# Kernel optimization log

Hardware: AMD Instinct MI355X
Metric: run time of the kernel (lower is better)

## Reference

```python
import jax, jax.numpy as jnp
import numpy as np

HEADS = 20
HEAD_DIM = 64  # 1280 // 20
NUM_STYLE_TOKENS = 4
FU_SCALE = 0.5
STYLE_SCALE = 1.0
SCALE = np.float32(1.0 / np.sqrt(HEAD_DIM))


def setup_inputs() -> dict:
    key = jax.random.key(0)
    ks = jax.random.split(key, 9)
    B, S, D_MODEL, D_CROSS, T = 4, 4096, 1280, 768, 77
    sd_m = np.float32(1.0 / np.sqrt(D_MODEL))
    sd_c = np.float32(1.0 / np.sqrt(D_CROSS))
    return {
        "hidden_states": jax.random.normal(ks[0], (B, S, D_MODEL), jnp.float32),
        "encoder_hidden_states": jax.random.normal(ks[1], (B, T + NUM_STYLE_TOKENS, D_CROSS), jnp.float32),
        "Wq": jax.random.normal(ks[2], (D_MODEL, D_MODEL), jnp.float32) * sd_m,
        "Wk": jax.random.normal(ks[3], (D_CROSS, D_MODEL), jnp.float32) * sd_c,
        "Wv": jax.random.normal(ks[4], (D_CROSS, D_MODEL), jnp.float32) * sd_c,
        "Wk_ip": jax.random.normal(ks[5], (D_CROSS, D_MODEL), jnp.float32) * sd_c,
        "Wv_ip": jax.random.normal(ks[6], (D_CROSS, D_MODEL), jnp.float32) * sd_c,
        "Wo": jax.random.normal(ks[7], (D_MODEL, D_MODEL), jnp.float32) * sd_m,
        "bo": jnp.zeros((D_MODEL,), jnp.float32),
    }


def _split_heads(x, B):
    # [B, L, H*D] -> [B, H, L, D]
    return x.reshape(B, -1, HEADS, HEAD_DIM).transpose(0, 2, 1, 3)


def _attn_blend(q, k, v):
    # Manual QK^T softmax with cross-batch prob blending (fuAttn / fuIPAttn).
    probs = jax.nn.softmax(jnp.einsum('bhsd,bhtd->bhst', q, k) * SCALE, axis=-1)
    probs = probs.at[1].set(FU_SCALE * probs[1] + (1.0 - FU_SCALE) * probs[0])
    probs = probs.at[3].set(FU_SCALE * probs[3] + (1.0 - FU_SCALE) * probs[2])
    return jnp.einsum('bhst,bhtd->bhsd', probs, v)


def reference(hidden_states, encoder_hidden_states, Wq, Wk, Wv, Wk_ip, Wv_ip, Wo, bo):
    B, S, _ = hidden_states.shape
    end_pos = encoder_hidden_states.shape[1] - NUM_STYLE_TOKENS
    text = encoder_hidden_states[:, :end_pos, :]       # [B, 77, Dc]
    ip_style = encoder_hidden_states[:, end_pos:, :]   # [B, 4, Dc]

    q = _split_heads(hidden_states @ Wq, B)   # [B,H,S,D]
    k = _split_heads(text @ Wk, B)            # [B,H,77,D]
    v = _split_heads(text @ Wv, B)

    hid = _attn_blend(q, k, v).transpose(0, 2, 1, 3).reshape(B, S, -1)
    raw = hid

    ip_k = _split_heads(ip_style @ Wk_ip, B)  # [B,H,4,D]
    ip_v = _split_heads(ip_style @ Wv_ip, B)
    ip_hid = _attn_blend(q, ip_k, ip_v).transpose(0, 2, 1, 3).reshape(B, S, -1)

    hid = hid + STYLE_SCALE * ip_hid
    # batch rows 0 and 2 keep the raw (text-only) attention output
    hid = hid.at[0].set(raw[0]).at[2].set(raw[2])

    return hid @ Wo + bo
```

## Files before the change

kernel.cpp:

```cpp
#include <hip/hip_runtime.h>
#include <hip/hip_bf16.h>

typedef _Float16 half8 __attribute__((ext_vector_type(8)));
typedef _Float16 half4 __attribute__((ext_vector_type(4)));
typedef float floatx4 __attribute__((ext_vector_type(4)));

#define HEADS_ 20
#define B_    4
#define S_    4096
#define DM    1280
#define DC    768
#define TTOK  77
#define NST   4
#define EROWS 81
#define MROWS 324
#define NT_K  20

__device__ inline void gload_lds16(const void* g, void* l) {
  __builtin_amdgcn_global_load_lds((const __attribute__((address_space(1))) void*)g,
                                   (__attribute__((address_space(3))) void*)l, 16, 0, 0);
}

__global__ __launch_bounds__(256) void cast_f16(const float* __restrict__ in,
                                                _Float16* __restrict__ out, long n) {
  long i = ((long)blockIdx.x * 256 + threadIdx.x) * 8L;
  long stride = (long)gridDim.x * 256 * 8;
  for (; i < n; i += stride) {
    float4 a = *(const float4*)(in + i);
    float4 b = *(const float4*)(in + i + 4);
    half8 h;
    h[0] = (_Float16)a.x; h[1] = (_Float16)a.y; h[2] = (_Float16)a.z; h[3] = (_Float16)a.w;
    h[4] = (_Float16)b.x; h[5] = (_Float16)b.y; h[6] = (_Float16)b.z; h[7] = (_Float16)b.w;
    *(half8*)(out + i) = h;
  }
}

struct TParams { const float* in[6]; _Float16* out[6]; int R[6]; };

__global__ __launch_bounds__(256) void transpose_cast6(TParams p) {
  const int z = blockIdx.z;
  const int R = p.R[z];
  const int r0 = blockIdx.y * 32, c0 = blockIdx.x * 32;
  if (r0 >= R) return;
  const float* __restrict__ in = p.in[z];
  _Float16* __restrict__ out = p.out[z];
  __shared__ float t[32][33];
  int tx = threadIdx.x & 31, ty = threadIdx.x >> 5;
  #pragma unroll
  for (int j = 0; j < 32; j += 8)
    t[ty + j][tx] = in[(size_t)(r0 + ty + j) * DM + c0 + tx];
  __syncthreads();
  #pragma unroll
  for (int j = 0; j < 32; j += 8)
    out[(size_t)(c0 + ty + j) * R + r0 + tx] = (_Float16)t[tx][ty + j];
}

struct Ptrs4 { const _Float16* B[4]; _Float16* C[4]; };

__global__ __launch_bounds__(256) void gemm_kv(const _Float16* __restrict__ A,
                                               Ptrs4 p4, int M, int K, int N) {
  const int tid = threadIdx.x, lane = tid & 63, w = tid >> 6;
  const _Float16* Bp = p4.B[blockIdx.z];
  _Float16* Ch = p4.C[blockIdx.z];
  const int bm = blockIdx.x, bn = blockIdx.y;

  __shared__ _Float16 As[128 * 32];
  __shared__ _Float16 Bs[128 * 32];

  const int wr = (w >> 1) * 64, wc = (w & 1) * 64;
  const int arow = wr + (lane & 15), brow = wc + (lane & 15);
  const int koff = (lane >> 4) * 8;
  floatx4 acc[4][4] = {};

  const int nk = K >> 5;
  for (int kt = 0; kt < nk; ++kt) {
    #pragma unroll
    for (int c = 0; c < 2; ++c) {
      int l16 = w * 64 + lane + c * 256;
      int row = l16 >> 2, kc = (l16 & 3) << 3;
      int gr = bm * 128 + row; if (gr > M - 1) gr = M - 1;
      gload_lds16(A + (size_t)gr * K + kt * 32 + kc, &As[(w + c * 4) * 512]);
      int grb = bn * 128 + row;
      gload_lds16(Bp + (size_t)grb * K + kt * 32 + kc, &Bs[(w + c * 4) * 512]);
    }
    __syncthreads();
    half8 af[4], bf[4];
    #pragma unroll
    for (int m = 0; m < 4; m++) af[m] = *(const half8*)&As[(arow + m * 16) * 32 + koff];
    #pragma unroll
    for (int n = 0; n < 4; n++) bf[n] = *(const half8*)&Bs[(brow + n * 16) * 32 + koff];
    #pragma unroll
    for (int m = 0; m < 4; m++)
      #pragma unroll
      for (int n = 0; n < 4; n++)
        acc[m][n] = __builtin_amdgcn_mfma_f32_16x16x32_f16(af[m], bf[n], acc[m][n], 0, 0, 0);
    __syncthreads();
  }

  const int r0 = (lane >> 4) * 4, c0 = lane & 15;
  #pragma unroll
  for (int m = 0; m < 4; m++) {
    #pragma unroll
    for (int r = 0; r < 4; r++) {
      int grow = bm * 128 + wr + m * 16 + r0 + r;
      if (grow >= M) continue;
      size_t base = (size_t)grow * N + bn * 128 + wc + c0;
      #pragma unroll
      for (int n = 0; n < 4; n++) Ch[base + n * 16] = (_Float16)acc[m][n][r];
    }
  }
}

template<int OMODE>
__global__ __launch_bounds__(256, 2)
void gemm8(const _Float16* __restrict__ A,
           const _Float16* __restrict__ B,
           void* __restrict__ Cout,
           const float* __restrict__ bias) {
  __shared__ _Float16 lds[36864];
  _Float16* const A0 = lds;
  _Float16* const A1 = lds + 8192;
  _Float16* const B0 = lds + 16384;
  _Float16* const B1 = lds + 26624;

  const int tid = threadIdx.x, lane = tid & 63, w = tid >> 6;
  const int swz = (blockIdx.x & 7) * 128 + (blockIdx.x >> 3);
  const int bm = swz >> 3, bn = swz & 7;

  const int wr = w >> 1, wc = w & 1;
  const int ql = lane & 15, lg = lane >> 4, xr = ql & 7;
  const int Abase = (wr * 64 + ql) * 64;
  const int Bbase = (wc * 80 + ql) * 64;

  const int srow = tid >> 3, sslot = tid & 7;
  const int scol = ((sslot ^ (srow & 7)) << 3);
  const _Float16* const Asrc = A + (size_t)(bm * 128 + srow) * DM + scol;
  const _Float16* const Bsrc = B + (size_t)(bn * 160 + srow) * DM + scol;
  const int ldst = w * 512;

  auto stage = [&](const _Float16* src, _Float16* buf, int q, int kt) {
    gload_lds16(src + (size_t)q * 32 * DM + kt * 64, buf + q * 2048 + ldst);
  };
  auto rdA = [&](const _Float16* buf, int m, int ks) -> half8 {
    return *(const half8*)(buf + Abase + m * 1024 + (((ks * 4 + lg) ^ xr) << 3));
  };
  auto rdB = [&](const _Float16* buf, int n, int ks) -> half8 {
    return *(const half8*)(buf + Bbase + n * 1024 + (((ks * 4 + lg) ^ xr) << 3));
  };

  floatx4 acc[4][5] = {};
  half8 bF[5], bG[5], aF[4], aG[4];

  #pragma unroll
  for (int q = 0; q < 4; ++q) stage(Asrc, A0, q, 0);
  #pragma unroll
  for (int q = 0; q < 5; ++q) stage(Bsrc, B0, q, 0);

  auto tile_body = [&](const _Float16* Ac, const _Float16* Bc,
                       _Float16* An, _Float16* Bn, int j, bool pref) {
    if (pref) {
      #pragma unroll
      for (int q = 0; q < 4; ++q) stage(Asrc, An, q, j + 1);
      #pragma unroll
      for (int q = 0; q < 5; ++q) stage(Bsrc, Bn, q, j + 1);
      asm volatile("s_waitcnt vmcnt(9)" ::: "memory");
    } else {
      asm volatile("s_waitcnt vmcnt(0)" ::: "memory");
    }
    asm volatile("s_waitcnt lgkmcnt(0)" ::: "memory");
    __builtin_amdgcn_sched_barrier(0);
    __builtin_amdgcn_s_barrier();
    __builtin_amdgcn_sched_barrier(0);

    #pragma unroll
    for (int n = 0; n < 5; ++n) bF[n] = rdB(Bc, n, 0);
    #pragma unroll
    for (int m = 0; m < 4; ++m) aF[m] = rdA(Ac, m, 0);
    #pragma unroll
    for (int m = 0; m < 4; ++m) {
      if (m == 0) { aG[0] = rdA(Ac, 0, 1); aG[1] = rdA(Ac, 1, 1); }
      if (m == 1) { aG[2] = rdA(Ac, 2, 1); aG[3] = rdA(Ac, 3, 1); bG[0] = rdB(Bc, 0, 1); }
      if (m == 2) { bG[1] = rdB(Bc, 1, 1); bG[2] = rdB(Bc, 2, 1); }
      if (m == 3) { bG[3] = rdB(Bc, 3, 1); bG[4] = rdB(Bc, 4, 1); }
      __builtin_amdgcn_s_setprio(1);
      #pragma unroll
      for (int n = 0; n < 5; ++n)
        acc[m][n] = __builtin_amdgcn_mfma_f32_16x16x32_f16(aF[m], bF[n], acc[m][n], 0, 0, 0);
      __builtin_amdgcn_s_setprio(0);
    }
    #pragma unroll
    for (int m = 0; m < 4; ++m) {
      __builtin_amdgcn_s_setprio(1);
      #pragma unroll
      for (int n = 0; n < 5; ++n)
        acc[m][n] = __builtin_amdgcn_mfma_f32_16x16x32_f16(aG[m], bG[n], acc[m][n], 0, 0, 0);
      __builtin_amdgcn_s_setprio(0);
    }
  };

  for (int j = 0; j < NT_K; j += 2) {
    tile_body(A0, B0, A1, B1, j, true);
    tile_body(A1, B1, A0, B0, j + 1, j + 2 < NT_K);
  }

  const int r0 = lg * 4;
  if constexpr (OMODE == 1) {
    _Float16* Ch = (_Float16*)Cout;
    #pragma unroll
    for (int m = 0; m < 4; ++m)
      #pragma unroll
      for (int r = 0; r < 4; ++r) {
        size_t base = (size_t)(bm * 128 + wr * 64 + m * 16 + r0 + r) * DM + bn * 160 + wc * 80 + ql;
        #pragma unroll
        for (int n = 0; n < 5; ++n)
          Ch[base + n * 16] = (_Float16)(acc[m][n][r] * 0.125f);
      }
  } else {
    float* Cf = (float*)Cout;
    float bv[5];
    #pragma unroll
    for (int n = 0; n < 5; ++n) bv[n] = bias[bn * 160 + wc * 80 + n * 16 + ql];
    #pragma unroll
    for (int m = 0; m < 4; ++m)
      #pragma unroll
      for (int r = 0; r < 4; ++r) {
        size_t base = (size_t)(bm * 128 + wr * 64 + m * 16 + r0 + r) * DM + bn * 160 + wc * 80 + ql;
        #pragma unroll
        for (int n = 0; n < 5; ++n)
          Cf[base + n * 16] = acc[m][n][r] + bv[n];
      }
  }
}

template<bool ODD>
__global__ __launch_bounds__(256) void attn_kernel(const _Float16* __restrict__ Q,
                                                   const _Float16* __restrict__ kf,
                                                   const _Float16* __restrict__ vf,
                                                   const _Float16* __restrict__ ipk,
                                                   const _Float16* __restrict__ ipv,
                                                   _Float16* __restrict__ hid) {
  const int tid = threadIdx.x;
  const int h = blockIdx.y;
  const int b = blockIdx.z * 2 + (ODD ? 1 : 0);
  constexpr bool odd = ODD;
  const int hoff = h * 64;
  const int lane = tid & 63, w = tid >> 6;
  const int g = lane >> 4, ql = lane & 15;

  __shared__ _Float16 K1s[96 * 64];
  __shared__ _Float16 K2s[ODD ? 96 * 64 : 8];
  __shared__ _Float16 VTs[64 * 104];
  __shared__ char Pl[4][16 * 208];
  char* const K1c = (char*)K1s;
  char* const K2c = (char*)K2s;
  char* const VTc = (char*)VTs;
  char* const Pwc = Pl[w];

  const half8 zero8 = {};
  for (int i = tid; i < 96 * 8; i += 256) {
    int key = i >> 3, hb = i & 7;
    int dst = (key * 128 + hb * 16) ^ ((key & 7) << 4);
    half8 v = zero8;
    if (key < TTOK)
      v = *(const half8*)(kf + (size_t)(b * EROWS + key) * DM + hoff + hb * 8);
    else if (odd && key >= 80 && key < 84)
      v = *(const half8*)(ipk + (size_t)(b * EROWS + key - 3) * DM + hoff + hb * 8);
    *(half8*)(K1c + dst) = v;
    if (odd) {
      half8 v2 = zero8;
      if (key < TTOK)
        v2 = *(const half8*)(kf + (size_t)((b - 1) * EROWS + key) * DM + hoff + hb * 8);
      else if (key >= 80 && key < 84)
        v2 = *(const half8*)(ipk + (size_t)((b - 1) * EROWS + key - 3) * DM + hoff + hb * 8);
      *(half8*)(K2c + dst) = v2;
    }
  }
  for (int i = tid; i < 96 * 8; i += 256) {
    int key = i >> 3, hb = i & 7;
    half8 v = zero8;
    if (key < TTOK)
      v = *(const half8*)(vf + (size_t)(b * EROWS + key) * DM + hoff + hb * 8);
    else if (odd && key >= 80 && key < 84)
      v = *(const half8*)(ipv + (size_t)(b * EROWS + key - 3) * DM + hoff + hb * 8);
    #pragma unroll
    for (int e = 0; e < 8; ++e) VTs[(hb * 8 + e) * 104 + key] = v[e];
  }
  __syncthreads();

  for (int t = 0; t < 4; ++t) {
    const int tq0 = blockIdx.x * 256 + t * 64 + w * 16;

    const _Float16* qp = Q + (size_t)(b * S_ + tq0 + ql) * DM + hoff + g * 8;
    half8 bq0 = *(const half8*)(qp);
    half8 bq1 = *(const half8*)(qp + 32);
    half8 bq20 = zero8, bq21 = zero8;
    if (odd) {
      const _Float16* qp2 = Q + (size_t)((b - 1) * S_ + tq0 + ql) * DM + hoff + g * 8;
      bq20 = *(const half8*)(qp2);
      bq21 = *(const half8*)(qp2 + 32);
    }

    floatx4 sA[6], sB[6];
    #pragma unroll
    for (int f = 0; f < (ODD ? 6 : 5); ++f) {
      int key = f * 16 + ql;
      int sw = (key & 7) << 4;
      half8 a0 = *(const half8*)(K1c + ((key * 128 + g * 16) ^ sw));
      half8 a1 = *(const half8*)(K1c + ((key * 128 + g * 16 + 64) ^ sw));
      floatx4 z = {};
      sA[f] = __builtin_amdgcn_mfma_f32_16x16x32_f16(a0, bq0, z, 0, 0, 0);
      sA[f] = __builtin_amdgcn_mfma_f32_16x16x32_f16(a1, bq1, sA[f], 0, 0, 0);
    }
    if (odd) {
      #pragma unroll
      for (int f = 0; f < 6; ++f) {
        int key = f * 16 + ql;
        int sw = (key & 7) << 4;
        half8 a0 = *(const half8*)(K2c + ((key * 128 + g * 16) ^ sw));
        half8 a1 = *(const half8*)(K2c + ((key * 128 + g * 16 + 64) ^ sw));
        floatx4 z = {};
        sB[f] = __builtin_amdgcn_mfma_f32_16x16x32_f16(a0, bq20, z, 0, 0, 0);
        sB[f] = __builtin_amdgcn_mfma_f32_16x16x32_f16(a1, bq21, sB[f], 0, 0, 0);
      }
    }

    const int kb = g * 4;
    float mA = -1e30f;
    #pragma unroll
    for (int f = 0; f < 4; ++f)
      #pragma unroll
      for (int r = 0; r < 4; ++r) mA = fmaxf(mA, sA[f][r]);
    #pragma unroll
    for (int r = 0; r < 4; ++r) if (kb + r <= 12) mA = fmaxf(mA, sA[4][r]);
    mA = fmaxf(mA, __shfl_xor(mA, 16));
    mA = fmaxf(mA, __shfl_xor(mA, 32));
    float lA = 0.f;
    #pragma unroll
    for (int f = 0; f < 4; ++f)
      #pragma unroll
      for (int r = 0; r < 4; ++r) { float e = __expf(sA[f][r] - mA); sA[f][r] = e; lA += e; }
    #pragma unroll
    for (int r = 0; r < 4; ++r) {
      float e = (kb + r <= 12) ? __expf(sA[4][r] - mA) : 0.f;
      sA[4][r] = e; lA += e;
    }
    lA += __shfl_xor(lA, 16);
    lA += __shfl_xor(lA, 32);

    float mB = -1e30f, lB = 0.f, invB = 0.f, invIpA = 0.f, invIpB = 0.f;
    if (odd) {
      #pragma unroll
      for (int f = 0; f < 4; ++f)
        #pragma unroll
        for (int r = 0; r < 4; ++r) mB = fmaxf(mB, sB[f][r]);
      #pragma unroll
      for (int r = 0; r < 4; ++r) if (kb + r <= 12) mB = fmaxf(mB, sB[4][r]);
      mB = fmaxf(mB, __shfl_xor(mB, 16));
      mB = fmaxf(mB, __shfl_xor(mB, 32));
      #pragma unroll
      for (int f = 0; f < 4; ++f)
        #pragma unroll
        for (int r = 0; r < 4; ++r) { float e = __expf(sB[f][r] - mB); sB[f][r] = e; lB += e; }
      #pragma unroll
      for (int r = 0; r < 4; ++r) {
        float e = (kb + r <= 12) ? __expf(sB[4][r] - mB) : 0.f;
        sB[4][r] = e; lB += e;
      }
      lB += __shfl_xor(lB, 16);
      lB += __shfl_xor(lB, 32);
      invB = 0.5f / lB;

      float mia = fmaxf(fmaxf(sA[5][0], sA[5][1]), fmaxf(sA[5][2], sA[5][3]));
      float mib = fmaxf(fmaxf(sB[5][0], sB[5][1]), fmaxf(sB[5][2], sB[5][3]));
      float lia = 0.f, lib = 0.f;
      #pragma unroll
      for (int r = 0; r < 4; ++r) {
        float ea = __expf(sA[5][r] - mia); sA[5][r] = ea; lia += ea;
        float eb = __expf(sB[5][r] - mib); sB[5][r] = eb; lib += eb;
      }
      invIpA = 0.5f / lia;
      invIpB = 0.5f / lib;
    }
    const float invA = (odd ? 0.5f : 1.0f) / lA;

    asm volatile("s_waitcnt lgkmcnt(0)" ::: "memory");
    __builtin_amdgcn_sched_barrier(0);
    #pragma unroll
    for (int f = 0; f < 6; ++f) {
      #pragma unroll
      for (int r = 0; r < 4; ++r) {
        int key = f * 16 + g * 4 + r;
        float p;
        if (f < 5) p = odd ? (sA[f][r] * invA + sB[f][r] * invB) : (sA[f][r] * invA);
        else p = (odd && g == 0) ? (sA[5][r] * invIpA + sB[5][r] * invIpB) : 0.f;
        *(_Float16*)(Pwc + ql * 208 + key * 2) = (_Float16)p;
      }
    }
    asm volatile("s_waitcnt lgkmcnt(0)" ::: "memory");
    __builtin_amdgcn_sched_barrier(0);

    half8 pf[3];
    #pragma unroll
    for (int kf2 = 0; kf2 < 3; ++kf2)
      pf[kf2] = *(const half8*)(Pwc + ql * 208 + g * 16 + kf2 * 64);
    floatx4 acc_o[4] = {};
    #pragma unroll
    for (int dt = 0; dt < 4; ++dt)
      #pragma unroll
      for (int kf2 = 0; kf2 < 3; ++kf2) {
        half8 vfr = *(const half8*)(VTc + (dt * 16 + ql) * 208 + g * 16 + kf2 * 64);
        acc_o[dt] = __builtin_amdgcn_mfma_f32_16x16x32_f16(vfr, pf[kf2], acc_o[dt], 0, 0, 0);
      }

    _Float16* hr = hid + (size_t)(b * S_ + tq0 + ql) * DM + hoff;
    #pragma unroll
    for (int dt = 0; dt < 4; ++dt) {
      half4 hv;
      #pragma unroll
      for (int r = 0; r < 4; ++r) hv[r] = (_Float16)acc_o[dt][r];
      *(half4*)(hr + dt * 16 + g * 4) = hv;
    }
  }
}

extern "C" void kernel_launch(void* const* d_in, const int* in_sizes, int n_in,
                              void* d_out, int out_size, void* d_ws, size_t ws_size,
                              hipStream_t stream) {
  const float* hs   = (const float*)d_in[0];
  const float* ehs  = (const float*)d_in[1];
  const float* Wq   = (const float*)d_in[2];
  const float* Wk   = (const float*)d_in[3];
  const float* Wv   = (const float*)d_in[4];
  const float* Wkip = (const float*)d_in[5];
  const float* Wvip = (const float*)d_in[6];
  const float* Wo   = (const float*)d_in[7];
  const float* bo   = (const float*)d_in[8];
  float* out = (float*)d_out;

  char* ws = (char*)d_ws;
  size_t off = 0;
  auto alloc = [&](size_t bytes) {
    void* p = ws + off;
    off += (bytes + 255) & ~(size_t)255;
    return p;
  };
  _Float16* hs16   = (_Float16*)alloc(20971520UL * 2);
  _Float16* ehs16  = (_Float16*)alloc(248832UL * 2);
  _Float16* WqT    = (_Float16*)alloc(1638400UL * 2);
  _Float16* WoT    = (_Float16*)alloc(1638400UL * 2);
  _Float16* WkT    = (_Float16*)alloc(983040UL * 2);
  _Float16* WvT    = (_Float16*)alloc(983040UL * 2);
  _Float16* WkipT  = (_Float16*)alloc(983040UL * 2);
  _Float16* WvipT  = (_Float16*)alloc(983040UL * 2);
  _Float16* Q16    = (_Float16*)alloc(20971520UL * 2);
  _Float16* kf16   = (_Float16*)alloc(324UL * 1280 * 2);
  _Float16* vf16   = (_Float16*)alloc(324UL * 1280 * 2);
  _Float16* ipkf16 = (_Float16*)alloc(324UL * 1280 * 2);
  _Float16* ipvf16 = (_Float16*)alloc(324UL * 1280 * 2);
  _Float16* hid16 = hs16;

  cast_f16<<<2048, 256, 0, stream>>>(hs, hs16, 20971520L);
  cast_f16<<<128, 256, 0, stream>>>(ehs, ehs16, 248832L);

  TParams tp;
  tp.in[0] = Wq;   tp.out[0] = WqT;   tp.R[0] = 1280;
  tp.in[1] = Wo;   tp.out[1] = WoT;   tp.R[1] = 1280;
  tp.in[2] = Wk;   tp.out[2] = WkT;   tp.R[2] = 768;
  tp.in[3] = Wv;   tp.out[3] = WvT;   tp.R[3] = 768;
  tp.in[4] = Wkip; tp.out[4] = WkipT; tp.R[4] = 768;
  tp.in[5] = Wvip; tp.out[5] = WvipT; tp.R[5] = 768;
  transpose_cast6<<<dim3(40, 40, 6), 256, 0, stream>>>(tp);

  Ptrs4 p4;
  p4.B[0] = WkT; p4.B[1] = WvT; p4.B[2] = WkipT; p4.B[3] = WvipT;
  p4.C[0] = kf16; p4.C[1] = vf16; p4.C[2] = ipkf16; p4.C[3] = ipvf16;

  gemm_kv<<<dim3(3, 10, 4), 256, 0, stream>>>(ehs16, p4, MROWS, DC, DM);
  gemm8<1><<<1024, 256, 0, stream>>>(hs16, WqT, (void*)Q16, nullptr);
  attn_kernel<false><<<dim3(16, 20, 2), 256, 0, stream>>>(Q16, kf16, vf16, ipkf16, ipvf16, hid16);
  attn_kernel<true><<<dim3(16, 20, 2), 256, 0, stream>>>(Q16, kf16, vf16, ipkf16, ipvf16, hid16);
  gemm8<2><<<1024, 256, 0, stream>>>(hid16, WoT, (void*)out, bo);
}
```

Measured before the change: 207.0 us.

## Reuse even-batch attention probabilities in odd-batch kernel via global buffer

```diff
diff --git a/kernel.cpp b/kernel.cpp
--- a/kernel.cpp
+++ b/kernel.cpp
@@ -238,21 +238,20 @@
                                                    const _Float16* __restrict__ vf,
                                                    const _Float16* __restrict__ ipk,
                                                    const _Float16* __restrict__ ipv,
+                                                   _Float16* __restrict__ P,
                                                    _Float16* __restrict__ hid) {
   const int tid = threadIdx.x;
   const int h = blockIdx.y;
-  const int b = blockIdx.z * 2 + (ODD ? 1 : 0);
-  constexpr bool odd = ODD;
+  const int pbz = blockIdx.z;
+  const int b = pbz * 2 + (ODD ? 1 : 0);
   const int hoff = h * 64;
   const int lane = tid & 63, w = tid >> 6;
   const int g = lane >> 4, ql = lane & 15;
 
   __shared__ _Float16 K1s[96 * 64];
-  __shared__ _Float16 K2s[ODD ? 96 * 64 : 8];
   __shared__ _Float16 VTs[64 * 104];
   __shared__ char Pl[4][16 * 208];
   char* const K1c = (char*)K1s;
-  char* const K2c = (char*)K2s;
   char* const VTc = (char*)VTs;
   char* const Pwc = Pl[w];
 
@@ -263,24 +262,16 @@
     half8 v = zero8;
     if (key < TTOK)
       v = *(const half8*)(kf + (size_t)(b * EROWS + key) * DM + hoff + hb * 8);
-    else if (odd && key >= 80 && key < 84)
+    else if (key >= 80 && key < 84)
       v = *(const half8*)(ipk + (size_t)(b * EROWS + key - 3) * DM + hoff + hb * 8);
     *(half8*)(K1c + dst) = v;
-    if (odd) {
-      half8 v2 = zero8;
-      if (key < TTOK)
-        v2 = *(const half8*)(kf + (size_t)((b - 1) * EROWS + key) * DM + hoff + hb * 8);
-      else if (key >= 80 && key < 84)
-        v2 = *(const half8*)(ipk + (size_t)((b - 1) * EROWS + key - 3) * DM + hoff + hb * 8);
-      *(half8*)(K2c + dst) = v2;
-    }
   }
   for (int i = tid; i < 96 * 8; i += 256) {
     int key = i >> 3, hb = i & 7;
     half8 v = zero8;
     if (key < TTOK)
       v = *(const half8*)(vf + (size_t)(b * EROWS + key) * DM + hoff + hb * 8);
-    else if (odd && key >= 80 && key < 84)
+    else if (ODD && key >= 80 && key < 84)
       v = *(const half8*)(ipv + (size_t)(b * EROWS + key - 3) * DM + hoff + hb * 8);
     #pragma unroll
     for (int e = 0; e < 8; ++e) VTs[(hb * 8 + e) * 104 + key] = v[e];
@@ -293,16 +284,10 @@
     const _Float16* qp = Q + (size_t)(b * S_ + tq0 + ql) * DM + hoff + g * 8;
     half8 bq0 = *(const half8*)(qp);
     half8 bq1 = *(const half8*)(qp + 32);
-    half8 bq20 = zero8, bq21 = zero8;
-    if (odd) {
-      const _Float16* qp2 = Q + (size_t)((b - 1) * S_ + tq0 + ql) * DM + hoff + g * 8;
-      bq20 = *(const half8*)(qp2);
-      bq21 = *(const half8*)(qp2 + 32);
-    }
-
-    floatx4 sA[6], sB[6];
-    #pragma unroll
-    for (int f = 0; f < (ODD ? 6 : 5); ++f) {
+
+    floatx4 sA[6];
+    #pragma unroll
+    for (int f = 0; f < 6; ++f) {
       int key = f * 16 + ql;
       int sw = (key & 7) << 4;
       half8 a0 = *(const half8*)(K1c + ((key * 128 + g * 16) ^ sw));
@@ -311,18 +296,6 @@
       sA[f] = __builtin_amdgcn_mfma_f32_16x16x32_f16(a0, bq0, z, 0, 0, 0);
       sA[f] = __builtin_amdgcn_mfma_f32_16x16x32_f16(a1, bq1, sA[f], 0, 0, 0);
     }
-    if (odd) {
-      #pragma unroll
-      for (int f = 0; f < 6; ++f) {
-        int key = f * 16 + ql;
-        int sw = (key & 7) << 4;
-        half8 a0 = *(const half8*)(K2c + ((key * 128 + g * 16) ^ sw));
-        half8 a1 = *(const half8*)(K2c + ((key * 128 + g * 16 + 64) ^ sw));
-        floatx4 z = {};
-        sB[f] = __builtin_amdgcn_mfma_f32_16x16x32_f16(a0, bq20, z, 0, 0, 0);
-        sB[f] = __builtin_amdgcn_mfma_f32_16x16x32_f16(a1, bq21, sB[f], 0, 0, 0);
-      }
-    }
 
     const int kb = g * 4;
     float mA = -1e30f;
@@ -346,42 +319,13 @@
     }
     lA += __shfl_xor(lA, 16);
     lA += __shfl_xor(lA, 32);
-
-    float mB = -1e30f, lB = 0.f, invB = 0.f, invIpA = 0.f, invIpB = 0.f;
-    if (odd) {
-      #pragma unroll
-      for (int f = 0; f < 4; ++f)
-        #pragma unroll
-        for (int r = 0; r < 4; ++r) mB = fmaxf(mB, sB[f][r]);
-      #pragma unroll
-      for (int r = 0; r < 4; ++r) if (kb + r <= 12) mB = fmaxf(mB, sB[4][r]);
-      mB = fmaxf(mB, __shfl_xor(mB, 16));
-      mB = fmaxf(mB, __shfl_xor(mB, 32));
-      #pragma unroll
-      for (int f = 0; f < 4; ++f)
-        #pragma unroll
-        for (int r = 0; r < 4; ++r) { float e = __expf(sB[f][r] - mB); sB[f][r] = e; lB += e; }
-      #pragma unroll
-      for (int r = 0; r < 4; ++r) {
-        float e = (kb + r <= 12) ? __expf(sB[4][r] - mB) : 0.f;
-        sB[4][r] = e; lB += e;
-      }
-      lB += __shfl_xor(lB, 16);
-      lB += __shfl_xor(lB, 32);
-      invB = 0.5f / lB;
-
-      float mia = fmaxf(fmaxf(sA[5][0], sA[5][1]), fmaxf(sA[5][2], sA[5][3]));
-      float mib = fmaxf(fmaxf(sB[5][0], sB[5][1]), fmaxf(sB[5][2], sB[5][3]));
-      float lia = 0.f, lib = 0.f;
-      #pragma unroll
-      for (int r = 0; r < 4; ++r) {
-        float ea = __expf(sA[5][r] - mia); sA[5][r] = ea; lia += ea;
-        float eb = __expf(sB[5][r] - mib); sB[5][r] = eb; lib += eb;
-      }
-      invIpA = 0.5f / lia;
-      invIpB = 0.5f / lib;
-    }
-    const float invA = (odd ? 0.5f : 1.0f) / lA;
+    const float invA = 1.0f / lA;
+
+    float mia = fmaxf(fmaxf(sA[5][0], sA[5][1]), fmaxf(sA[5][2], sA[5][3]));
+    float lia = 0.f;
+    #pragma unroll
+    for (int r = 0; r < 4; ++r) { float e = __expf(sA[5][r] - mia); sA[5][r] = e; lia += e; }
+    const float invIpA = 1.0f / lia;
 
     asm volatile("s_waitcnt lgkmcnt(0)" ::: "memory");
     __builtin_amdgcn_sched_barrier(0);
@@ -391,8 +335,8 @@
       for (int r = 0; r < 4; ++r) {
         int key = f * 16 + g * 4 + r;
         float p;
-        if (f < 5) p = odd ? (sA[f][r] * invA + sB[f][r] * invB) : (sA[f][r] * invA);
-        else p = (odd && g == 0) ? (sA[5][r] * invIpA + sB[5][r] * invIpB) : 0.f;
+        if (f < 5) p = sA[f][r] * invA;
+        else p = (g == 0) ? (sA[5][r] * invIpA) : 0.f;
         *(_Float16*)(Pwc + ql * 208 + key * 2) = (_Float16)p;
       }
     }
@@ -403,6 +347,21 @@
     #pragma unroll
     for (int kf2 = 0; kf2 < 3; ++kf2)
       pf[kf2] = *(const half8*)(Pwc + ql * 208 + g * 16 + kf2 * 64);
+
+    _Float16* const Pg = P + (((size_t)pbz * HEADS_ + h) * S_ + tq0 + ql) * 96 + g * 8;
+    if constexpr (!ODD) {
+      #pragma unroll
+      for (int kf2 = 0; kf2 < 3; ++kf2)
+        *(half8*)(Pg + kf2 * 32) = pf[kf2];
+    } else {
+      half8 pe[3];
+      #pragma unroll
+      for (int kf2 = 0; kf2 < 3; ++kf2) pe[kf2] = *(const half8*)(Pg + kf2 * 32);
+      #pragma unroll
+      for (int kf2 = 0; kf2 < 3; ++kf2)
+        pf[kf2] = (pf[kf2] + pe[kf2]) * (_Float16)0.5f;
+    }
+
     floatx4 acc_o[4] = {};
     #pragma unroll
     for (int dt = 0; dt < 4; ++dt)
@@ -457,6 +416,7 @@
   _Float16* vf16   = (_Float16*)alloc(324UL * 1280 * 2);
   _Float16* ipkf16 = (_Float16*)alloc(324UL * 1280 * 2);
   _Float16* ipvf16 = (_Float16*)alloc(324UL * 1280 * 2);
+  _Float16* Pbuf   = (_Float16*)alloc(2UL * HEADS_ * S_ * 96 * 2);
   _Float16* hid16 = hs16;
 
   cast_f16<<<2048, 256, 0, stream>>>(hs, hs16, 20971520L);
@@ -477,7 +437,7 @@
 
   gemm_kv<<<dim3(3, 10, 4), 256, 0, stream>>>(ehs16, p4, MROWS, DC, DM);
   gemm8<1><<<1024, 256, 0, stream>>>(hs16, WqT, (void*)Q16, nullptr);
-  attn_kernel<false><<<dim3(16, 20, 2), 256, 0, stream>>>(Q16, kf16, vf16, ipkf16, ipvf16, hid16);
-  attn_kernel<true><<<dim3(16, 20, 2), 256, 0, stream>>>(Q16, kf16, vf16, ipkf16, ipvf16, hid16);
+  attn_kernel<false><<<dim3(16, 20, 2), 256, 0, stream>>>(Q16, kf16, vf16, ipkf16, ipvf16, Pbuf, hid16);
+  attn_kernel<true><<<dim3(16, 20, 2), 256, 0, stream>>>(Q16, kf16, vf16, ipkf16, ipvf16, Pbuf, hid16);
   gemm8<2><<<1024, 256, 0, stream>>>(hid16, WoT, (void*)out, bo);
 }
```

After: 206.8 us. No clear change (-0.1%).
